# Optimization experiments

Hardware: AMD Instinct MI355X
Metric: run time of the kernel (lower is better)

## Reference

```python
import jax, jax.numpy as jnp
import numpy as np


def gru_cell(x, h, wi, wh, bi, bh):
    # torch.nn.GRUCell math
    gi = x @ wi.T + bi  # (B, 3*H)
    gh = h @ wh.T + bh
    i_r, i_z, i_n = jnp.split(gi, 3, axis=-1)
    h_r, h_z, h_n = jnp.split(gh, 3, axis=-1)
    r = jax.nn.sigmoid(i_r + h_r)
    z = jax.nn.sigmoid(i_z + h_z)
    n = jnp.tanh(i_n + r * h_n)
    return (1.0 - z) * n + z * h


def setup_inputs() -> dict:
    key = jax.random.key(0)
    B, T = 256, 512
    dim_ctx, dim_mel, r = 512, 160, 2
    dim_pre, dim_att = 128, 256
    dim_rnn = dim_att + dim_ctx  # 768
    ks = jax.random.split(key, 32)
    rn = lambda k, shp, s=0.05: jax.random.normal(k, shp, jnp.float32) * s
    w = jax.random.uniform(ks[1], (B, T), jnp.float32)
    w = w / jnp.sum(w, axis=1, keepdims=True)  # valid attention distribution
    return {
        "x": rn(ks[0], (B, r, dim_mel // r), 1.0),
        "w": w,
        "h_att": jnp.zeros((B, dim_att), jnp.float32),
        "h_dec0": jnp.zeros((B, dim_rnn), jnp.float32),
        "h_dec1": jnp.zeros((B, dim_rnn), jnp.float32),
        "memory": rn(ks[2], (B, T, dim_ctx), 1.0),
        # PreNet: Linear(dim_mel->dim_pre)+ReLU, Linear(dim_pre->dim_pre)+ReLU
        "pre_w1": rn(ks[3], (dim_pre, dim_mel)), "pre_b1": rn(ks[4], (dim_pre,)),
        "pre_w2": rn(ks[5], (dim_pre, dim_pre)), "pre_b2": rn(ks[6], (dim_pre,)),
        # attention GRUCell (dim_pre -> dim_att)
        "att_wi": rn(ks[7], (3 * dim_att, dim_pre)), "att_wh": rn(ks[8], (3 * dim_att, dim_att)),
        "att_bi": rn(ks[9], (3 * dim_att,)), "att_bh": rn(ks[10], (3 * dim_att,)),
        # ContentMarkovAttention query projection (dim_att -> dim_ctx)
        "q_w": rn(ks[11], (dim_ctx, dim_att)), "q_b": rn(ks[12], (dim_ctx,)),
        # ResGRUCell 0 (dim_rnn -> dim_rnn)
        "dec0_wi": rn(ks[13], (3 * dim_rnn, dim_rnn)), "dec0_wh": rn(ks[14], (3 * dim_rnn, dim_rnn)),
        "dec0_bi": rn(ks[15], (3 * dim_rnn,)), "dec0_bh": rn(ks[16], (3 * dim_rnn,)),
        # ResGRUCell 1
        "dec1_wi": rn(ks[17], (3 * dim_rnn, dim_rnn)), "dec1_wh": rn(ks[18], (3 * dim_rnn, dim_rnn)),
        "dec1_bi": rn(ks[19], (3 * dim_rnn,)), "dec1_bh": rn(ks[20], (3 * dim_rnn,)),
    }


def reference(x, w, h_att, h_dec0, h_dec1, memory,
              pre_w1, pre_b1, pre_w2, pre_b2,
              att_wi, att_wh, att_bi, att_bh,
              q_w, q_b,
              dec0_wi, dec0_wh, dec0_bi, dec0_bh,
              dec1_wi, dec1_wh, dec1_bi, dec1_bh):
    B = x.shape[0]
    # PreNet on flattened r*mel frames
    xf = x.reshape(B, -1)
    h = jax.nn.relu(xf @ pre_w1.T + pre_b1)
    h = jax.nn.relu(h @ pre_w2.T + pre_b2)  # (B, dim_pre)
    # context vector with PREVIOUS attention weights (matches bmm before update)
    ctx = jnp.einsum('bt,btc->bc', w, memory)
    # attention GRU
    h_att_new = gru_cell(h, h_att, att_wi, att_wh, att_bi, att_bh)
    # ContentMarkovAttention: content scores * Markov (stay/move) prior, renormalized
    q = h_att_new @ q_w.T + q_b  # (B, dim_ctx)
    e = jnp.einsum('btc,bc->bt', memory, q) / jnp.sqrt(jnp.float32(memory.shape[-1]))
    a = jax.nn.softmax(e, axis=-1)
    w_shift = jnp.concatenate([jnp.zeros_like(w[:, :1]), w[:, :-1]], axis=1)
    w_prior = 0.5 * (w + w_shift)
    w_new = a * w_prior
    w_new = w_new / (jnp.sum(w_new, axis=1, keepdims=True) + 1e-8)
    # stacked residual GRU cells on [h_att; ctx]
    x_dec = jnp.concatenate([h_att_new, ctx], axis=1)  # (B, dim_rnn)
    h0 = gru_cell(x_dec, h_dec0, dec0_wi, dec0_wh, dec0_bi, dec0_bh) + x_dec
    h1 = gru_cell(h0, h_dec1, dec1_wi, dec1_wh, dec1_bi, dec1_bh) + h0
    return h1, w_new, h_att_new, h0, h1
```

## Files before the change

kernel.cpp:

```cpp
#include <hip/hip_runtime.h>
#include <math.h>

#define B    256
#define T    512
#define CTX  512
#define MEL  160
#define PRE  128
#define ATT  256
#define RNN  768
#define G3   2304

typedef __attribute__((ext_vector_type(8))) short short8;
typedef __attribute__((ext_vector_type(4))) float f32x4;

__device__ __forceinline__ unsigned short f2bf(float f) {
    unsigned u = __float_as_uint(f);
    unsigned r = (u + 0x7fffu + ((u >> 16) & 1u)) >> 16;
    return (unsigned short)r;
}
__device__ __forceinline__ float bf2f(unsigned short h) {
    return __uint_as_float((unsigned)h << 16);
}

__device__ __forceinline__ void conv8(const float* p, short8* hi8, short8* lo8) {
    const float4 v0 = *(const float4*)p;
    const float4 v1 = *(const float4*)(p + 4);
    const float av[8] = {v0.x, v0.y, v0.z, v0.w, v1.x, v1.y, v1.z, v1.w};
    short hi[8], lo[8];
    #pragma unroll
    for (int u = 0; u < 8; ++u) {
        const unsigned short h = f2bf(av[u]);
        hi[u] = (short)h;
        lo[u] = (short)f2bf(av[u] - bf2f(h));
    }
    *hi8 = *(const short8*)hi;
    *lo8 = *(const short8*)lo;
}

__global__ void wconv_kernel(const float* __restrict__ pw1, const float* __restrict__ pw2,
                             const float* __restrict__ wi, const float* __restrict__ wh,
                             const float* __restrict__ qw,
                             short* __restrict__ p1h, short* __restrict__ p1l,
                             short* __restrict__ p2h, short* __restrict__ p2l,
                             short* __restrict__ wih, short* __restrict__ wil,
                             short* __restrict__ whh, short* __restrict__ whl,
                             short* __restrict__ qwh, short* __restrict__ qwl) {
    int s = blockIdx.x * 256 + threadIdx.x;
    const float* src; short *dh, *dl; int K, KS, slot;
    if (s < 2560)                       { src = pw1; dh = p1h; dl = p1l; K = MEL; KS = 5; slot = s; }
    else if ((s -= 2560) < 2048)        { src = pw2; dh = p2h; dl = p2l; K = PRE; KS = 4; slot = s; }
    else if ((s -= 2048) < 12288)       { src = wi;  dh = wih; dl = wil; K = PRE; KS = 4; slot = s; }
    else if ((s -= 12288) < 24576)      { src = wh;  dh = whh; dl = whl; K = ATT; KS = 8; slot = s; }
    else if ((s -= 24576) < 16384)      { src = qw;  dh = qwh; dl = qwl; K = ATT; KS = 8; slot = s; }
    else return;
    const int lane = slot & 63;
    const int ks = (slot >> 6) % KS;
    const int nt = (slot >> 6) / KS;
    const int n = nt * 16 + (lane & 15);
    const int k = ks * 32 + (lane >> 4) * 8;
    conv8(src + (size_t)n * K + k, (short8*)(dh + (size_t)slot * 8), (short8*)(dl + (size_t)slot * 8));
}

__global__ __launch_bounds__(512) void front_mfma_kernel(
        const float* __restrict__ x, const float* __restrict__ b1,
        const float* __restrict__ b2, const float* __restrict__ h_att,
        const float* __restrict__ bi, const float* __restrict__ bh,
        const float* __restrict__ qb,
        const short* __restrict__ p1h, const short* __restrict__ p1l,
        const short* __restrict__ p2h, const short* __restrict__ p2l,
        const short* __restrict__ wih, const short* __restrict__ wil,
        const short* __restrict__ whh, const short* __restrict__ whl,
        const short* __restrict__ qwh, const short* __restrict__ qwl,
        float* __restrict__ h_att_out, float* __restrict__ x_dec,
        float* __restrict__ q) {
    __shared__ __align__(16) short AH[8][64][8];
    __shared__ __align__(16) short AL[8][64][8];
    __shared__ __align__(16) float S[16][RNN];
    __shared__ __align__(16) float S2[16][RNN];
    __shared__ __align__(16) float hs[16][ATT];

    const int tid = threadIdx.x;
    const int wave = tid >> 6, lane = tid & 63;
    const int mb = blockIdx.x * 16;
    const int col = lane & 15, rowq = lane >> 4;

    for (int i = tid; i < 16 * ATT; i += 512)
        hs[i >> 8][i & 255] = h_att[(size_t)(mb + (i >> 8)) * ATT + (i & 255)];
    if (tid < 320) {
        const int sub = tid >> 6, ln = tid & 63;
        const int row = ln & 15, kk = sub * 32 + (ln >> 4) * 8;
        conv8(x + (size_t)(mb + row) * MEL + kk, (short8*)AH[sub][ln], (short8*)AL[sub][ln]);
    }
    __syncthreads();

    {
        const int nt = wave;
        f32x4 acc = {0.f, 0.f, 0.f, 0.f};
        #pragma unroll
        for (int ks = 0; ks < 5; ++ks) {
            const short8 a_h = *(const short8*)AH[ks][lane];
            const short8 a_l = *(const short8*)AL[ks][lane];
            const size_t fo = ((size_t)(nt * 5 + ks) * 64 + lane) * 8;
            const short8 b_h = *(const short8*)(p1h + fo);
            const short8 b_l = *(const short8*)(p1l + fo);
            acc = __builtin_amdgcn_mfma_f32_16x16x32_bf16(a_h, b_h, acc, 0, 0, 0);
            acc = __builtin_amdgcn_mfma_f32_16x16x32_bf16(a_l, b_h, acc, 0, 0, 0);
            acc = __builtin_amdgcn_mfma_f32_16x16x32_bf16(a_h, b_l, acc, 0, 0, 0);
        }
        const int j = nt * 16 + col;
        const float bb = b1[j];
        #pragma unroll
        for (int r = 0; r < 4; ++r)
            S[rowq * 4 + r][j] = fmaxf(acc[r] + bb, 0.f);
    }
    __syncthreads();
    if (tid < 256) {
        const int sub = tid >> 6, ln = tid & 63;
        const int row = ln & 15, kk = sub * 32 + (ln >> 4) * 8;
        conv8(&S[row][kk], (short8*)AH[sub][ln], (short8*)AL[sub][ln]);
    }
    __syncthreads();

    {
        const int nt = wave;
        f32x4 acc = {0.f, 0.f, 0.f, 0.f};
        #pragma unroll
        for (int ks = 0; ks < 4; ++ks) {
            const short8 a_h = *(const short8*)AH[ks][lane];
            const short8 a_l = *(const short8*)AL[ks][lane];
            const size_t fo = ((size_t)(nt * 4 + ks) * 64 + lane) * 8;
            const short8 b_h = *(const short8*)(p2h + fo);
            const short8 b_l = *(const short8*)(p2l + fo);
            acc = __builtin_amdgcn_mfma_f32_16x16x32_bf16(a_h, b_h, acc, 0, 0, 0);
            acc = __builtin_amdgcn_mfma_f32_16x16x32_bf16(a_l, b_h, acc, 0, 0, 0);
            acc = __builtin_amdgcn_mfma_f32_16x16x32_bf16(a_h, b_l, acc, 0, 0, 0);
        }
        const int j = wave * 16 + col;
        const float bb = b2[j];
        #pragma unroll
        for (int r = 0; r < 4; ++r)
            S[rowq * 4 + r][j] = fmaxf(acc[r] + bb, 0.f);
    }
    __syncthreads();
    if (tid < 256) {
        const int sub = tid >> 6, ln = tid & 63;
        const int row = ln & 15, kk = sub * 32 + (ln >> 4) * 8;
        conv8(&S[row][kk], (short8*)AH[sub][ln], (short8*)AL[sub][ln]);
    }
    __syncthreads();

    for (int t = 0; t < 6; ++t) {
        const int nt = wave * 6 + t;
        f32x4 acc = {0.f, 0.f, 0.f, 0.f};
        #pragma unroll
        for (int ks = 0; ks < 4; ++ks) {
            const short8 a_h = *(const short8*)AH[ks][lane];
            const short8 a_l = *(const short8*)AL[ks][lane];
            const size_t fo = ((size_t)(nt * 4 + ks) * 64 + lane) * 8;
            const short8 b_h = *(const short8*)(wih + fo);
            const short8 b_l = *(const short8*)(wil + fo);
            acc = __builtin_amdgcn_mfma_f32_16x16x32_bf16(a_h, b_h, acc, 0, 0, 0);
            acc = __builtin_amdgcn_mfma_f32_16x16x32_bf16(a_l, b_h, acc, 0, 0, 0);
            acc = __builtin_amdgcn_mfma_f32_16x16x32_bf16(a_h, b_l, acc, 0, 0, 0);
        }
        const int j = nt * 16 + col;
        #pragma unroll
        for (int r = 0; r < 4; ++r) S[rowq * 4 + r][j] = acc[r];
    }
    __syncthreads();
    {
        const int sub = tid >> 6, ln = tid & 63;
        const int row = ln & 15, kk = sub * 32 + (ln >> 4) * 8;
        conv8(&hs[row][kk], (short8*)AH[sub][ln], (short8*)AL[sub][ln]);
    }
    __syncthreads();

    for (int t = 0; t < 6; ++t) {
        const int nt = wave * 6 + t;
        f32x4 acc = {0.f, 0.f, 0.f, 0.f};
        #pragma unroll
        for (int ks = 0; ks < 8; ++ks) {
            const short8 a_h = *(const short8*)AH[ks][lane];
            const short8 a_l = *(const short8*)AL[ks][lane];
            const size_t fo = ((size_t)(nt * 8 + ks) * 64 + lane) * 8;
            const short8 b_h = *(const short8*)(whh + fo);
            const short8 b_l = *(const short8*)(whl + fo);
            acc = __builtin_amdgcn_mfma_f32_16x16x32_bf16(a_h, b_h, acc, 0, 0, 0);
            acc = __builtin_amdgcn_mfma_f32_16x16x32_bf16(a_l, b_h, acc, 0, 0, 0);
            acc = __builtin_amdgcn_mfma_f32_16x16x32_bf16(a_h, b_l, acc, 0, 0, 0);
        }
        const int j = nt * 16 + col;
        #pragma unroll
        for (int r = 0; r < 4; ++r) S2[rowq * 4 + r][j] = acc[r];
    }
    __syncthreads();

    for (int e = tid; e < 16 * ATT; e += 512) {
        const int b = e >> 8, j = e & 255;
        const float ir = S[b][j] + bi[j];
        const float iz = S[b][ATT + j] + bi[ATT + j];
        const float in_ = S[b][2 * ATT + j] + bi[2 * ATT + j];
        const float hr = S2[b][j] + bh[j];
        const float hz = S2[b][ATT + j] + bh[ATT + j];
        const float hn = S2[b][2 * ATT + j] + bh[2 * ATT + j];
        const float r = 1.f / (1.f + expf(-(ir + hr)));
        const float z = 1.f / (1.f + expf(-(iz + hz)));
        const float n = tanhf(in_ + r * hn);
        const float hnew = (1.f - z) * n + z * hs[b][j];
        h_att_out[(size_t)(mb + b) * ATT + j] = hnew;
        x_dec[(size_t)(mb + b) * RNN + j] = hnew;
        hs[b][j] = hnew;
    }
    __syncthreads();
    {
        const int sub = tid >> 6, ln = tid & 63;
        const int row = ln & 15, kk = sub * 32 + (ln >> 4) * 8;
        conv8(&hs[row][kk], (short8*)AH[sub][ln], (short8*)AL[sub][ln]);
    }
    __syncthreads();

    for (int t = 0; t < 4; ++t) {
        const int nt = wave * 4 + t;
        f32x4 acc = {0.f, 0.f, 0.f, 0.f};
        #pragma unroll
        for (int ks = 0; ks < 8; ++ks) {
            const short8 a_h = *(const short8*)AH[ks][lane];
            const short8 a_l = *(const short8*)AL[ks][lane];
            const size_t fo = ((size_t)(nt * 8 + ks) * 64 + lane) * 8;
            const short8 b_h = *(const short8*)(qwh + fo);
            const short8 b_l = *(const short8*)(qwl + fo);
            acc = __builtin_amdgcn_mfma_f32_16x16x32_bf16(a_h, b_h, acc, 0, 0, 0);
            acc = __builtin_amdgcn_mfma_f32_16x16x32_bf16(a_l, b_h, acc, 0, 0, 0);
            acc = __builtin_amdgcn_mfma_f32_16x16x32_bf16(a_h, b_l, acc, 0, 0, 0);
        }
        const int j = nt * 16 + col;
        const float bb = qb[j];
        #pragma unroll
        for (int r = 0; r < 4; ++r)
            q[(size_t)(mb + rowq * 4 + r) * CTX + j] = acc[r] + bb;
    }
}

__global__ void mempass_kernel(const float* __restrict__ mem, const float* __restrict__ w,
                               const float* __restrict__ q, float* __restrict__ e,
                               float* __restrict__ ctx_part) {
    const int b = blockIdx.y, slice = blockIdx.x;
    const int tid = threadIdx.x;
    const int wave = tid >> 6, lane = tid & 63;
    __shared__ float qs[CTX];
    __shared__ float ctx_s[4][CTX];
    for (int i = tid; i < CTX; i += 256) qs[i] = q[(size_t)b * CTX + i];
    __syncthreads();

    const int c0 = lane * 4;
    const int c1 = 256 + lane * 4;
    const float q0 = qs[c0], q1 = qs[c0 + 1], q2 = qs[c0 + 2], q3 = qs[c0 + 3];
    const float q4 = qs[c1], q5 = qs[c1 + 1], q6 = qs[c1 + 2], q7 = qs[c1 + 3];

    const float* mb = mem + (size_t)b * T * CTX;
    float acc[8] = {0.f, 0.f, 0.f, 0.f, 0.f, 0.f, 0.f, 0.f};
    const float invs = 0.04419417382415922f;
    const int t0 = slice * 64 + wave * 16;

    #pragma unroll 4
    for (int i = 0; i < 16; ++i) {
        const int t = t0 + i;
        const float* row = mb + (size_t)t * CTX;
        const float4 m0 = *(const float4*)(row + c0);
        const float4 m1 = *(const float4*)(row + c1);
        const float wt = w[(size_t)b * T + t];
        float ep = m0.x * q0 + m0.y * q1 + m0.z * q2 + m0.w * q3
                 + m1.x * q4 + m1.y * q5 + m1.z * q6 + m1.w * q7;
        #pragma unroll
        for (int off = 32; off; off >>= 1) ep += __shfl_xor(ep, off);
        if (lane == 0) e[(size_t)b * T + t] = ep * invs;
        acc[0] += wt * m0.x; acc[1] += wt * m0.y; acc[2] += wt * m0.z; acc[3] += wt * m0.w;
        acc[4] += wt * m1.x; acc[5] += wt * m1.y; acc[6] += wt * m1.z; acc[7] += wt * m1.w;
    }
    ctx_s[wave][c0] = acc[0]; ctx_s[wave][c0 + 1] = acc[1]; ctx_s[wave][c0 + 2] = acc[2]; ctx_s[wave][c0 + 3] = acc[3];
    ctx_s[wave][c1] = acc[4]; ctx_s[wave][c1 + 1] = acc[5]; ctx_s[wave][c1 + 2] = acc[6]; ctx_s[wave][c1 + 3] = acc[7];
    __syncthreads();
    for (int c = tid; c < CTX; c += 256) {
        const float s = ctx_s[0][c] + ctx_s[1][c] + ctx_s[2][c] + ctx_s[3][c];
        ctx_part[((size_t)slice * B + b) * CTX + c] = s;
    }
}

__global__ void mid_kernel(const float* __restrict__ part, float* __restrict__ x_dec,
                           const float* __restrict__ e, const float* __restrict__ w,
                           float* __restrict__ w_new) {
    const int tid = threadIdx.x;
    if (blockIdx.x < 512) {
        const int idx = blockIdx.x * 256 + tid;
        const int b = idx >> 9, c = idx & 511;
        float s = 0.f;
        #pragma unroll
        for (int sl = 0; sl < 8; ++sl) s += part[((size_t)sl * B + b) * CTX + c];
        x_dec[(size_t)b * RNN + ATT + c] = s;
        return;
    }
    const int b = blockIdx.x - 512;
    const int lane = tid & 63, wv = tid >> 6;
    __shared__ float red[4];
    const float* eb = e + (size_t)b * T;
    const float* wb = w + (size_t)b * T;
    const float e0 = eb[tid], e1 = eb[tid + 256];

    float m = fmaxf(e0, e1);
    #pragma unroll
    for (int o = 32; o; o >>= 1) m = fmaxf(m, __shfl_xor(m, o));
    if (lane == 0) red[wv] = m;
    __syncthreads();
    m = fmaxf(fmaxf(red[0], red[1]), fmaxf(red[2], red[3]));
    __syncthreads();

    const float x0 = expf(e0 - m), x1 = expf(e1 - m);
    float s = x0 + x1;
    #pragma unroll
    for (int o = 32; o; o >>= 1) s += __shfl_xor(s, o);
    if (lane == 0) red[wv] = s;
    __syncthreads();
    s = red[0] + red[1] + red[2] + red[3];
    __syncthreads();

    const float p0 = 0.5f * (wb[tid] + (tid > 0 ? wb[tid - 1] : 0.f));
    const float p1 = 0.5f * (wb[tid + 256] + wb[tid + 255]);
    const float m0 = (x0 / s) * p0;
    const float m1 = (x1 / s) * p1;
    float s2 = m0 + m1;
    #pragma unroll
    for (int o = 32; o; o >>= 1) s2 += __shfl_xor(s2, o);
    if (lane == 0) red[wv] = s2;
    __syncthreads();
    s2 = red[0] + red[1] + red[2] + red[3];
    const float inv = 1.f / (s2 + 1e-8f);
    w_new[(size_t)b * T + tid] = m0 * inv;
    w_new[(size_t)b * T + tid + 256] = m1 * inv;
}

__global__ __launch_bounds__(256) void mfma_gemm_kernel(
        const float* __restrict__ Agi, const float* __restrict__ Agh,
        const float* __restrict__ Wgi, const float* __restrict__ Wgh,
        float* __restrict__ Cgi, float* __restrict__ Cgh) {
    const int mat = blockIdx.z;
    const float* __restrict__ A = mat ? Agh : Agi;
    const float* __restrict__ W = mat ? Wgh : Wgi;
    float* __restrict__ C = mat ? Cgh : Cgi;

    const int m0 = blockIdx.y * 64;
    const int n0 = blockIdx.x * 64;

    __shared__ __align__(16) short AH[4096];
    __shared__ __align__(16) short AL[4096];
    __shared__ __align__(16) short WH[4096];
    __shared__ __align__(16) short WL[4096];

    const int tid = threadIdx.x;
    const int lane = tid & 63;
    const int wave = tid >> 6;
    const int wm = wave >> 1, wn = wave & 1;

    f32x4 acc[2][2] = {{{0.f, 0.f, 0.f, 0.f}, {0.f, 0.f, 0.f, 0.f}},
                       {{0.f, 0.f, 0.f, 0.f}, {0.f, 0.f, 0.f, 0.f}}};

    for (int k0 = 0; k0 < RNN; k0 += 64) {
        #pragma unroll
        for (int si = 0; si < 2; ++si) {
            const int s = tid + si * 256;
            const int sub = s >> 6;
            const int ln = s & 63;
            const int row = (sub >> 1) * 16 + (ln & 15);
            const int kk = (sub & 1) * 32 + (ln >> 4) * 8;
            conv8(A + (size_t)(m0 + row) * RNN + k0 + kk,
                  (short8*)&AH[s * 8], (short8*)&AL[s * 8]);
            conv8(W + (size_t)(n0 + row) * RNN + k0 + kk,
                  (short8*)&WH[s * 8], (short8*)&WL[s * 8]);
        }
        __syncthreads();

        #pragma unroll
        for (int ks = 0; ks < 2; ++ks) {
            short8 ah[2], al[2], wh[2], wl[2];
            #pragma unroll
            for (int i = 0; i < 2; ++i) {
                const int asub = ((wm * 2 + i) * 2 + ks);
                ah[i] = *(const short8*)&AH[(asub * 64 + lane) * 8];
                al[i] = *(const short8*)&AL[(asub * 64 + lane) * 8];
                const int wsub = ((wn * 2 + i) * 2 + ks);
                wh[i] = *(const short8*)&WH[(wsub * 64 + lane) * 8];
                wl[i] = *(const short8*)&WL[(wsub * 64 + lane) * 8];
            }
            #pragma unroll
            for (int i = 0; i < 2; ++i)
                #pragma unroll
                for (int j = 0; j < 2; ++j) {
                    acc[i][j] = __builtin_amdgcn_mfma_f32_16x16x32_bf16(ah[i], wh[j], acc[i][j], 0, 0, 0);
                    acc[i][j] = __builtin_amdgcn_mfma_f32_16x16x32_bf16(al[i], wh[j], acc[i][j], 0, 0, 0);
                    acc[i][j] = __builtin_amdgcn_mfma_f32_16x16x32_bf16(ah[i], wl[j], acc[i][j], 0, 0, 0);
                }
        }
        __syncthreads();
    }

    const int rowq = lane >> 4, col = lane & 15;
    #pragma unroll
    for (int i = 0; i < 2; ++i)
        #pragma unroll
        for (int j = 0; j < 2; ++j) {
            const int rbase = m0 + wm * 32 + i * 16 + rowq * 4;
            const int cidx = n0 + wn * 32 + j * 16 + col;
            #pragma unroll
            for (int r = 0; r < 4; ++r)
                C[(size_t)(rbase + r) * G3 + cidx] = acc[i][j][r];
        }
}

__global__ void gru_res_kernel(const float* __restrict__ gi, const float* __restrict__ gh,
                               const float* __restrict__ x_in, const float* __restrict__ h_prev,
                               const float* __restrict__ bi, const float* __restrict__ bh,
                               float* __restrict__ out0, float* __restrict__ out1) {
    const int idx = blockIdx.x * 256 + threadIdx.x;
    const int b = idx / RNN, j = idx % RNN;
    const float* gib = gi + (size_t)b * G3;
    const float* ghb = gh + (size_t)b * G3;
    const float ir = gib[j] + bi[j];
    const float iz = gib[RNN + j] + bi[RNN + j];
    const float in_ = gib[2 * RNN + j] + bi[2 * RNN + j];
    const float hr = ghb[j] + bh[j];
    const float hz = ghb[RNN + j] + bh[RNN + j];
    const float hn = ghb[2 * RNN + j] + bh[2 * RNN + j];
    const float r = 1.f / (1.f + expf(-(ir + hr)));
    const float z = 1.f / (1.f + expf(-(iz + hz)));
    const float n = tanhf(in_ + r * hn);
    const float res = (1.f - z) * n + z * h_prev[idx] + x_in[idx];
    out0[idx] = res;
    if (out1) out1[idx] = res;
}

extern "C" void kernel_launch(void* const* d_in, const int* in_sizes, int n_in,
                              void* d_out, int out_size, void* d_ws, size_t ws_size,
                              hipStream_t stream) {
    const float* x       = (const float*)d_in[0];
    const float* w       = (const float*)d_in[1];
    const float* h_att   = (const float*)d_in[2];
    const float* h_dec0  = (const float*)d_in[3];
    const float* h_dec1  = (const float*)d_in[4];
    const float* memory  = (const float*)d_in[5];
    const float* pre_w1  = (const float*)d_in[6];
    const float* pre_b1  = (const float*)d_in[7];
    const float* pre_w2  = (const float*)d_in[8];
    const float* pre_b2  = (const float*)d_in[9];
    const float* att_wi  = (const float*)d_in[10];
    const float* att_wh  = (const float*)d_in[11];
    const float* att_bi  = (const float*)d_in[12];
    const float* att_bh  = (const float*)d_in[13];
    const float* q_w     = (const float*)d_in[14];
    const float* q_b     = (const float*)d_in[15];
    const float* dec0_wi = (const float*)d_in[16];
    const float* dec0_wh = (const float*)d_in[17];
    const float* dec0_bi = (const float*)d_in[18];
    const float* dec0_bh = (const float*)d_in[19];
    const float* dec1_wi = (const float*)d_in[20];
    const float* dec1_wh = (const float*)d_in[21];
    const float* dec1_bi = (const float*)d_in[22];
    const float* dec1_bh = (const float*)d_in[23];

    float* out = (float*)d_out;
    float* o_h1a = out;
    float* o_wn  = out + 196608;
    float* o_ha  = out + 327680;
    float* o_h0  = out + 393216;
    float* o_h1b = out + 589824;

    float* ws    = (float*)d_ws;
    float* q     = ws;
    float* e     = ws + 131072;
    float* x_dec = ws + 262144;
    float* ctxp  = ws + 458752;
    float* gi    = ws + 1507328;
    float* gh    = ws + 2097152;
    short* sb    = (short*)(ws + 2686976);
    short* p1h = sb;             short* p1l = sb + 20480;
    short* p2h = sb + 40960;     short* p2l = sb + 57344;
    short* wih = sb + 73728;     short* wil = sb + 172032;
    short* whh = sb + 270336;    short* whl = sb + 466944;
    short* qwh = sb + 663552;    short* qwl = sb + 794624;

    wconv_kernel<<<226, 256, 0, stream>>>(pre_w1, pre_w2, att_wi, att_wh, q_w,
                                          p1h, p1l, p2h, p2l, wih, wil, whh, whl, qwh, qwl);
    front_mfma_kernel<<<16, 512, 0, stream>>>(x, pre_b1, pre_b2, h_att, att_bi, att_bh, q_b,
                                              p1h, p1l, p2h, p2l, wih, wil, whh, whl, qwh, qwl,
                                              o_ha, x_dec, q);
    mempass_kernel<<<dim3(8, B), 256, 0, stream>>>(memory, w, q, e, ctxp);
    mid_kernel<<<768, 256, 0, stream>>>(ctxp, x_dec, e, w, o_wn);

    mfma_gemm_kernel<<<dim3(G3 / 64, B / 64, 2), 256, 0, stream>>>(
        x_dec, h_dec0, dec0_wi, dec0_wh, gi, gh);
    gru_res_kernel<<<768, 256, 0, stream>>>(gi, gh, x_dec, h_dec0, dec0_bi, dec0_bh, o_h0, nullptr);

    mfma_gemm_kernel<<<dim3(G3 / 64, B / 64, 2), 256, 0, stream>>>(
        o_h0, h_dec1, dec1_wi, dec1_wh, gi, gh);
    gru_res_kernel<<<768, 256, 0, stream>>>(gi, gh, o_h0, h_dec1, dec1_bi, dec1_bh, o_h1a, o_h1b);
}
```

Before: 161.9 us.

## Fuse memory pass, context reduction and attention softmax into one kernel per batch

Replaces the split mempass kernel (8 slices per batch row, partial context sums written to global) and the separate mid kernel with a single 1024-thread block per batch row. Each block streams its whole memory row, keeps scores and attention weights in shared memory, reduces the context across 16 waves, and computes the softmax and Markov-prior renormalisation in place. This removes one launch and the global round trips for partial contexts and scores. In exchange the grid drops from 2048 blocks to 256 large blocks with about 36KB of shared memory each, which may reduce the parallelism available to hide latency on the memory-bound stream.

```diff
diff --git a/kernel.cpp b/kernel.cpp
--- a/kernel.cpp
+++ b/kernel.cpp
@@ -241,15 +241,22 @@
     }
 }
 
-__global__ void mempass_kernel(const float* __restrict__ mem, const float* __restrict__ w,
-                               const float* __restrict__ q, float* __restrict__ e,
-                               float* __restrict__ ctx_part) {
-    const int b = blockIdx.y, slice = blockIdx.x;
+__global__ __launch_bounds__(1024) void attn_kernel(
+        const float* __restrict__ mem, const float* __restrict__ w,
+        const float* __restrict__ q, float* __restrict__ x_dec,
+        float* __restrict__ w_new) {
+    __shared__ float qs[CTX];
+    __shared__ float ws_[T];
+    __shared__ float e_s[T];
+    __shared__ float ctx_s[16][CTX];
+    __shared__ float red[16];
+
+    const int b = blockIdx.x;
     const int tid = threadIdx.x;
     const int wave = tid >> 6, lane = tid & 63;
-    __shared__ float qs[CTX];
-    __shared__ float ctx_s[4][CTX];
-    for (int i = tid; i < CTX; i += 256) qs[i] = q[(size_t)b * CTX + i];
+
+    if (tid < CTX) qs[tid] = q[(size_t)b * CTX + tid];
+    else ws_[tid - CTX] = w[(size_t)b * T + tid - CTX];
     __syncthreads();
 
     const int c0 = lane * 4;
@@ -260,82 +267,64 @@
     const float* mb = mem + (size_t)b * T * CTX;
     float acc[8] = {0.f, 0.f, 0.f, 0.f, 0.f, 0.f, 0.f, 0.f};
     const float invs = 0.04419417382415922f;
-    const int t0 = slice * 64 + wave * 16;
+    const int t0 = wave * 32;
 
     #pragma unroll 4
-    for (int i = 0; i < 16; ++i) {
+    for (int i = 0; i < 32; ++i) {
         const int t = t0 + i;
         const float* row = mb + (size_t)t * CTX;
         const float4 m0 = *(const float4*)(row + c0);
         const float4 m1 = *(const float4*)(row + c1);
-        const float wt = w[(size_t)b * T + t];
+        const float wt = ws_[t];
         float ep = m0.x * q0 + m0.y * q1 + m0.z * q2 + m0.w * q3
                  + m1.x * q4 + m1.y * q5 + m1.z * q6 + m1.w * q7;
         #pragma unroll
         for (int off = 32; off; off >>= 1) ep += __shfl_xor(ep, off);
-        if (lane == 0) e[(size_t)b * T + t] = ep * invs;
+        if (lane == 0) e_s[t] = ep * invs;
         acc[0] += wt * m0.x; acc[1] += wt * m0.y; acc[2] += wt * m0.z; acc[3] += wt * m0.w;
         acc[4] += wt * m1.x; acc[5] += wt * m1.y; acc[6] += wt * m1.z; acc[7] += wt * m1.w;
     }
     ctx_s[wave][c0] = acc[0]; ctx_s[wave][c0 + 1] = acc[1]; ctx_s[wave][c0 + 2] = acc[2]; ctx_s[wave][c0 + 3] = acc[3];
     ctx_s[wave][c1] = acc[4]; ctx_s[wave][c1 + 1] = acc[5]; ctx_s[wave][c1 + 2] = acc[6]; ctx_s[wave][c1 + 3] = acc[7];
     __syncthreads();
-    for (int c = tid; c < CTX; c += 256) {
-        const float s = ctx_s[0][c] + ctx_s[1][c] + ctx_s[2][c] + ctx_s[3][c];
-        ctx_part[((size_t)slice * B + b) * CTX + c] = s;
-    }
-}
-
-__global__ void mid_kernel(const float* __restrict__ part, float* __restrict__ x_dec,
-                           const float* __restrict__ e, const float* __restrict__ w,
-                           float* __restrict__ w_new) {
-    const int tid = threadIdx.x;
-    if (blockIdx.x < 512) {
-        const int idx = blockIdx.x * 256 + tid;
-        const int b = idx >> 9, c = idx & 511;
+
+    if (tid < CTX) {
         float s = 0.f;
         #pragma unroll
-        for (int sl = 0; sl < 8; ++sl) s += part[((size_t)sl * B + b) * CTX + c];
-        x_dec[(size_t)b * RNN + ATT + c] = s;
-        return;
-    }
-    const int b = blockIdx.x - 512;
-    const int lane = tid & 63, wv = tid >> 6;
-    __shared__ float red[4];
-    const float* eb = e + (size_t)b * T;
-    const float* wb = w + (size_t)b * T;
-    const float e0 = eb[tid], e1 = eb[tid + 256];
-
-    float m = fmaxf(e0, e1);
+        for (int wv = 0; wv < 16; ++wv) s += ctx_s[wv][tid];
+        x_dec[(size_t)b * RNN + ATT + tid] = s;
+    }
+
+    const bool act = (tid < T);
+    float ev = act ? e_s[tid] : -1e30f;
+    float m = ev;
     #pragma unroll
     for (int o = 32; o; o >>= 1) m = fmaxf(m, __shfl_xor(m, o));
-    if (lane == 0) red[wv] = m;
-    __syncthreads();
-    m = fmaxf(fmaxf(red[0], red[1]), fmaxf(red[2], red[3]));
-    __syncthreads();
-
-    const float x0 = expf(e0 - m), x1 = expf(e1 - m);
-    float s = x0 + x1;
+    if (act && lane == 0) red[wave] = m;
+    __syncthreads();
+    m = red[0];
+    #pragma unroll
+    for (int wv = 1; wv < 8; ++wv) m = fmaxf(m, red[wv]);
+    __syncthreads();
+
+    const float x0 = act ? expf(ev - m) : 0.f;
+    float s = x0;
     #pragma unroll
     for (int o = 32; o; o >>= 1) s += __shfl_xor(s, o);
-    if (lane == 0) red[wv] = s;
-    __syncthreads();
-    s = red[0] + red[1] + red[2] + red[3];
-    __syncthreads();
-
-    const float p0 = 0.5f * (wb[tid] + (tid > 0 ? wb[tid - 1] : 0.f));
-    const float p1 = 0.5f * (wb[tid + 256] + wb[tid + 255]);
-    const float m0 = (x0 / s) * p0;
-    const float m1 = (x1 / s) * p1;
-    float s2 = m0 + m1;
+    if (act && lane == 0) red[wave] = s;
+    __syncthreads();
+    s = red[0] + red[1] + red[2] + red[3] + red[4] + red[5] + red[6] + red[7];
+    __syncthreads();
+
+    const float p = act ? 0.5f * (ws_[tid] + (tid > 0 ? ws_[tid - 1] : 0.f)) : 0.f;
+    const float m0v = (x0 / s) * p;
+    float s2 = m0v;
     #pragma unroll
     for (int o = 32; o; o >>= 1) s2 += __shfl_xor(s2, o);
-    if (lane == 0) red[wv] = s2;
-    __syncthreads();
-    s2 = red[0] + red[1] + red[2] + red[3];
-    const float inv = 1.f / (s2 + 1e-8f);
-    w_new[(size_t)b * T + tid] = m0 * inv;
-    w_new[(size_t)b * T + tid + 256] = m1 * inv;
+    if (act && lane == 0) red[wave] = s2;
+    __syncthreads();
+    s2 = red[0] + red[1] + red[2] + red[3] + red[4] + red[5] + red[6] + red[7];
+    if (act) w_new[(size_t)b * T + tid] = m0v / (s2 + 1e-8f);
 }
 
 __global__ __launch_bounds__(256) void mfma_gemm_kernel(
@@ -474,12 +463,10 @@
 
     float* ws    = (float*)d_ws;
     float* q     = ws;
-    float* e     = ws + 131072;
-    float* x_dec = ws + 262144;
-    float* ctxp  = ws + 458752;
-    float* gi    = ws + 1507328;
-    float* gh    = ws + 2097152;
-    short* sb    = (short*)(ws + 2686976);
+    float* x_dec = ws + 131072;
+    float* gi    = ws + 327680;
+    float* gh    = ws + 917504;
+    short* sb    = (short*)(ws + 1507328);
     short* p1h = sb;             short* p1l = sb + 20480;
     short* p2h = sb + 40960;     short* p2l = sb + 57344;
     short* wih = sb + 73728;     short* wil = sb + 172032;
@@ -491,8 +478,7 @@
     front_mfma_kernel<<<16, 512, 0, stream>>>(x, pre_b1, pre_b2, h_att, att_bi, att_bh, q_b,
                                               p1h, p1l, p2h, p2l, wih, wil, whh, whl, qwh, qwl,
                                               o_ha, x_dec, q);
-    mempass_kernel<<<dim3(8, B), 256, 0, stream>>>(memory, w, q, e, ctxp);
-    mid_kernel<<<768, 256, 0, stream>>>(ctxp, x_dec, e, w, o_wn);
+    attn_kernel<<<B, 1024, 0, stream>>>(memory, w, q, x_dec, o_wn);
 
     mfma_gemm_kernel<<<dim3(G3 / 64, B / 64, 2), 256, 0, stream>>>(
         x_dec, h_dec0, dec0_wi, dec0_wh, gi, gh);
```

Measured after the change: 155.3 us. 1.04x faster.
